# Kernel optimization log

Hardware: AMD Instinct MI355X
Metric: run time of the kernel (lower is better)

The kernel has to match this reference:

```python
import jax, jax.numpy as jnp
import numpy as np

N, K, DC, DH = 50000, 32, 64, 64  # nodes, neighbors, dim_c(+dim_h), dim_hidden

def setup_inputs() -> dict:
    key = jax.random.key(0)
    ks = jax.random.split(key, 8)
    return {
        "z":     jax.random.normal(ks[0], (N, DC), dtype=jnp.float32),
        "z_":    jax.random.normal(ks[1], (N, K, DC), dtype=jnp.float32),
        "W_cur": jax.random.normal(ks[2], (DC, DH), dtype=jnp.float32) * 0.1,
        "b_cur": jax.random.uniform(ks[3], (DH,), minval=-0.1, maxval=0.1, dtype=jnp.float32),
        "W_nbr": jax.random.normal(ks[4], (2 * DC, DH), dtype=jnp.float32) * 0.1,
        "b_nbr": jax.random.uniform(ks[5], (DH,), minval=-0.1, maxval=0.1, dtype=jnp.float32),
        "W_out": jax.random.normal(ks[6], (2 * DH, DC), dtype=jnp.float32) * 0.1,
        "b_out": jax.random.uniform(ks[7], (DC,), minval=-0.1, maxval=0.1, dtype=jnp.float32),
    }

def reference(z, z_, W_cur, b_cur, W_nbr, b_nbr, W_out, b_out):
    # cur branch: CELU(Linear(z))  -> [N, DH]
    v = jax.nn.celu(z @ W_cur + b_cur)
    # nbr branch: concat(self expanded over nbr axis, neighbors) -> [N, K, 2*DC]
    zz = jnp.concatenate((jnp.broadcast_to(z[:, None, :], z_.shape), z_), axis=-1)
    # CELU(Linear) then sum over neighbor axis -> [N, DH]
    v_ = jax.nn.celu(zz @ W_nbr + b_nbr).sum(axis=-2)
    # final linear on concatenated features -> [N, DC]
    dc = jnp.concatenate((v, v_), axis=-1) @ W_out + b_out
    return dc
```

## Files before the change

### kernel.cpp

```cpp
#include <hip/hip_runtime.h>
#include <hip/hip_bf16.h>

typedef float  f32x16 __attribute__((ext_vector_type(16)));
typedef short  bf16x8 __attribute__((ext_vector_type(8)));

__device__ __forceinline__ unsigned short f2bf(float x) {
  union { float f; unsigned u; } v; v.f = x;
  return (unsigned short)((v.u + 0x7FFFu + ((v.u >> 16) & 1u)) >> 16);
}

__device__ __forceinline__ float celu1(float x) {
  return x > 0.f ? x : (__expf(x) - 1.f);
}

struct Stage { float4 z[4][2]; float4 a[4][2]; };

__device__ __forceinline__ void issue_stage(Stage& s, const float* __restrict__ zptr,
                                            const float* __restrict__ aptr, int lo, int hi) {
#pragma unroll
  for (int ks = 0; ks < 4; ++ks) {
    const float* pz = zptr + ks * 16 + 8 * hi;
    s.z[ks][0] = *reinterpret_cast<const float4*>(pz);
    s.z[ks][1] = *reinterpret_cast<const float4*>(pz + 4);
    const float* pa = aptr + lo * 64 + ks * 16 + 8 * hi;
    s.a[ks][0] = *reinterpret_cast<const float4*>(pa);
    s.a[ks][1] = *reinterpret_cast<const float4*>(pa + 4);
  }
}

__device__ __forceinline__ bf16x8 to_frag(float4 a, float4 b) {
  bf16x8 r;
  r[0] = (short)f2bf(a.x); r[1] = (short)f2bf(a.y);
  r[2] = (short)f2bf(a.z); r[3] = (short)f2bf(a.w);
  r[4] = (short)f2bf(b.x); r[5] = (short)f2bf(b.y);
  r[6] = (short)f2bf(b.z); r[7] = (short)f2bf(b.w);
  return r;
}

__device__ __forceinline__ bf16x8 ldsfrag(const unsigned short* w, int S, int col, int k0) {
  return *reinterpret_cast<const bf16x8*>(w + col * S + (k0 ^ ((col & 7) << 3)));
}

__global__ __launch_bounds__(256, 2) void gcu_kernel(
    const float* __restrict__ z, const float* __restrict__ z_,
    const float* __restrict__ Wc, const float* __restrict__ bc,
    const float* __restrict__ Wn, const float* __restrict__ bn,
    const float* __restrict__ Wo, const float* __restrict__ bo,
    float* __restrict__ out, int N) {
  __shared__ __align__(16) unsigned short sWnT[64 * 128];
  __shared__ __align__(16) unsigned short sWcT[64 * 64];
  __shared__ __align__(16) unsigned short sWoT[64 * 128];
  __shared__ __align__(16) unsigned short sVV[4][32 * 128];

  const int tid = threadIdx.x;
  for (int i = tid; i < 128 * 64; i += 256) {
    int c = i & 63, k = i >> 6;
    int d = c * 128 + (k ^ ((c & 7) << 3));
    sWnT[d] = f2bf(Wn[i]);
    sWoT[d] = f2bf(Wo[i]);
  }
  for (int i = tid; i < 64 * 64; i += 256) {
    int c = i & 63, k = i >> 6;
    sWcT[c * 64 + (k ^ ((c & 7) << 3))] = f2bf(Wc[i]);
  }
  __syncthreads();

  const int wid = tid >> 6, lane = tid & 63;
  const int lo = lane & 31, hi = lane >> 5;
  const int base = (blockIdx.x * 4 + wid) * 32;
  if (base >= N) return;

  unsigned short* vv = &sVV[wid][0];
  const float bn0 = bn[lo], bn1 = bn[32 + lo];
  const float bc0 = bc[lo], bc1 = bc[32 + lo];
  const float bo0 = bo[lo], bo1 = bo[32 + lo];

  auto node_ptrs = [&](int n, const float*& zp, const float*& ap) {
    int nl = min(base + n, N - 1);
    zp = z + (size_t)nl * 64;
    ap = z_ + (size_t)nl * 2048;
  };

  auto process = [&](const Stage& s, int n) {
    f32x16 acc0{}, acc1{};
#pragma unroll
    for (int ks = 0; ks < 8; ++ks) {
      bf16x8 af = (ks < 4) ? to_frag(s.z[ks][0], s.z[ks][1])
                           : to_frag(s.a[ks - 4][0], s.a[ks - 4][1]);
      bf16x8 b0 = ldsfrag(sWnT, 128, lo,      ks * 16 + 8 * hi);
      bf16x8 b1 = ldsfrag(sWnT, 128, lo + 32, ks * 16 + 8 * hi);
      acc0 = __builtin_amdgcn_mfma_f32_32x32x16_bf16(af, b0, acc0, 0, 0, 0);
      acc1 = __builtin_amdgcn_mfma_f32_32x32x16_bf16(af, b1, acc1, 0, 0, 0);
    }
    float s0 = 0.f, s1 = 0.f;
#pragma unroll
    for (int r = 0; r < 16; ++r) {
      s0 += celu1(acc0[r] + bn0);
      s1 += celu1(acc1[r] + bn1);
    }
    s0 += __shfl_xor(s0, 32, 64);
    s1 += __shfl_xor(s1, 32, 64);
    if (hi == 0) {
      vv[n * 128 + ((64 + lo) ^ ((n & 7) << 3))] = f2bf(s0);
      vv[n * 128 + ((96 + lo) ^ ((n & 7) << 3))] = f2bf(s1);
    }
  };

  Stage sA, sB;
  { const float *zp, *ap; node_ptrs(0, zp, ap); issue_stage(sA, zp, ap, lo, hi); }
#pragma unroll 1
  for (int nn = 0; nn < 32; nn += 2) {
    const float *zp, *ap;
    node_ptrs(nn + 1, zp, ap);
    issue_stage(sB, zp, ap, lo, hi);
    process(sA, nn);
    node_ptrs(nn + 2, zp, ap);
    issue_stage(sA, zp, ap, lo, hi);
    process(sB, nn + 1);
  }

  {
    f32x16 a0{}, a1{};
    int nl = min(base + lo, N - 1);
    const float* zp = z + (size_t)nl * 64;
#pragma unroll
    for (int ks = 0; ks < 4; ++ks) {
      float4 x0 = *reinterpret_cast<const float4*>(zp + ks * 16 + 8 * hi);
      float4 x1 = *reinterpret_cast<const float4*>(zp + ks * 16 + 8 * hi + 4);
      bf16x8 af = to_frag(x0, x1);
      bf16x8 b0 = ldsfrag(sWcT, 64, lo,      ks * 16 + 8 * hi);
      bf16x8 b1 = ldsfrag(sWcT, 64, lo + 32, ks * 16 + 8 * hi);
      a0 = __builtin_amdgcn_mfma_f32_32x32x16_bf16(af, b0, a0, 0, 0, 0);
      a1 = __builtin_amdgcn_mfma_f32_32x32x16_bf16(af, b1, a1, 0, 0, 0);
    }
#pragma unroll
    for (int r = 0; r < 16; ++r) {
      int row = (r & 3) + 8 * (r >> 2) + 4 * hi;
      vv[row * 128 + ( lo        ^ ((row & 7) << 3))] = f2bf(celu1(a0[r] + bc0));
      vv[row * 128 + ((32 + lo)  ^ ((row & 7) << 3))] = f2bf(celu1(a1[r] + bc1));
    }
  }

  {
    f32x16 a0{}, a1{};
#pragma unroll
    for (int ks = 0; ks < 8; ++ks) {
      bf16x8 af = *reinterpret_cast<const bf16x8*>(
          vv + lo * 128 + ((ks * 16 + 8 * hi) ^ ((lo & 7) << 3)));
      bf16x8 b0 = ldsfrag(sWoT, 128, lo,      ks * 16 + 8 * hi);
      bf16x8 b1 = ldsfrag(sWoT, 128, lo + 32, ks * 16 + 8 * hi);
      a0 = __builtin_amdgcn_mfma_f32_32x32x16_bf16(af, b0, a0, 0, 0, 0);
      a1 = __builtin_amdgcn_mfma_f32_32x32x16_bf16(af, b1, a1, 0, 0, 0);
    }
#pragma unroll
    for (int r = 0; r < 16; ++r) {
      int row = base + (r & 3) + 8 * (r >> 2) + 4 * hi;
      if (row < N) {
        out[(size_t)row * 64 + lo]      = a0[r] + bo0;
        out[(size_t)row * 64 + 32 + lo] = a1[r] + bo1;
      }
    }
  }
}

extern "C" void kernel_launch(void* const* d_in, const int* in_sizes, int n_in,
                              void* d_out, int out_size, void* d_ws, size_t ws_size,
                              hipStream_t stream) {
  const float* z  = (const float*)d_in[0];
  const float* z_ = (const float*)d_in[1];
  const float* Wc = (const float*)d_in[2];
  const float* bc = (const float*)d_in[3];
  const float* Wn = (const float*)d_in[4];
  const float* bn = (const float*)d_in[5];
  const float* Wo = (const float*)d_in[6];
  const float* bo = (const float*)d_in[7];
  float* out = (float*)d_out;
  const int N = in_sizes[0] / 64;
  const int tasks = (N + 31) / 32;
  const int blocks = (tasks + 3) / 4;
  gcu_kernel<<<blocks, 256, 0, stream>>>(z, z_, Wc, bc, Wn, bn, Wo, bo, out, N);
}
```

Baseline: 109.3 us.

## Halve nodes per wave, shrink LDS, stage z in LDS, read Wc/Wo from global

Each wave now handles 16 nodes instead of 32, and launch bounds ask for three blocks per CU instead of two. To make room, only the neighbor weight stays in LDS, and the per-wave feature buffer is halved. The self features z are converted to bf16 once and staged in LDS, where both the neighbor GEMM and the cur branch read them. Wc and Wo fragments are now gathered straight from global memory with strided scalar loads. This cuts LDS use and per-thread staging registers to raise occupancy on the bandwidth-bound z_ stream. The cost is twice as many blocks, each repeating the Wn setup, plus uncoalesced global weight reads and half-used 32-row MFMA tiles in the final stages.

```diff
diff --git a/kernel.cpp b/kernel.cpp
--- a/kernel.cpp
+++ b/kernel.cpp
@@ -13,15 +13,12 @@
   return x > 0.f ? x : (__expf(x) - 1.f);
 }
 
-struct Stage { float4 z[4][2]; float4 a[4][2]; };
+struct Stage { float4 a[4][2]; };
 
-__device__ __forceinline__ void issue_stage(Stage& s, const float* __restrict__ zptr,
-                                            const float* __restrict__ aptr, int lo, int hi) {
+__device__ __forceinline__ void issue_stage(Stage& s, const float* __restrict__ aptr,
+                                            int lo, int hi) {
 #pragma unroll
   for (int ks = 0; ks < 4; ++ks) {
-    const float* pz = zptr + ks * 16 + 8 * hi;
-    s.z[ks][0] = *reinterpret_cast<const float4*>(pz);
-    s.z[ks][1] = *reinterpret_cast<const float4*>(pz + 4);
     const float* pa = aptr + lo * 64 + ks * 16 + 8 * hi;
     s.a[ks][0] = *reinterpret_cast<const float4*>(pa);
     s.a[ks][1] = *reinterpret_cast<const float4*>(pa + 4);
@@ -41,52 +38,67 @@
   return *reinterpret_cast<const bf16x8*>(w + col * S + (k0 ^ ((col & 7) << 3)));
 }
 
-__global__ __launch_bounds__(256, 2) void gcu_kernel(
+__device__ __forceinline__ bf16x8 wfrag(const float* __restrict__ W, int ld, int col, int k0) {
+  bf16x8 f;
+#pragma unroll
+  for (int j = 0; j < 8; ++j) f[j] = (short)f2bf(W[(size_t)(k0 + j) * ld + col]);
+  return f;
+}
+
+__global__ __launch_bounds__(256, 3) void gcu_kernel(
     const float* __restrict__ z, const float* __restrict__ z_,
     const float* __restrict__ Wc, const float* __restrict__ bc,
     const float* __restrict__ Wn, const float* __restrict__ bn,
     const float* __restrict__ Wo, const float* __restrict__ bo,
     float* __restrict__ out, int N) {
   __shared__ __align__(16) unsigned short sWnT[64 * 128];
-  __shared__ __align__(16) unsigned short sWcT[64 * 64];
-  __shared__ __align__(16) unsigned short sWoT[64 * 128];
-  __shared__ __align__(16) unsigned short sVV[4][32 * 128];
+  __shared__ __align__(16) unsigned short sVV[4][16 * 128];
 
   const int tid = threadIdx.x;
+  const int wid = tid >> 6, lane = tid & 63;
+  const int lo = lane & 31, hi = lane >> 5;
+  const int base = (blockIdx.x * 4 + wid) * 16;
+  unsigned short* vv = &sVV[wid][0];
+
   for (int i = tid; i < 128 * 64; i += 256) {
     int c = i & 63, k = i >> 6;
-    int d = c * 128 + (k ^ ((c & 7) << 3));
-    sWnT[d] = f2bf(Wn[i]);
-    sWoT[d] = f2bf(Wo[i]);
+    sWnT[c * 128 + (k ^ ((c & 7) << 3))] = f2bf(Wn[i]);
   }
-  for (int i = tid; i < 64 * 64; i += 256) {
-    int c = i & 63, k = i >> 6;
-    sWcT[c * 64 + (k ^ ((c & 7) << 3))] = f2bf(Wc[i]);
+
+  if (base < N) {
+    int r = lane >> 2, seg = lane & 3;
+    int node = min(base + r, N - 1);
+    const float* src = z + (size_t)node * 64 + seg * 16;
+    float4 x0 = *reinterpret_cast<const float4*>(src);
+    float4 x1 = *reinterpret_cast<const float4*>(src + 4);
+    float4 x2 = *reinterpret_cast<const float4*>(src + 8);
+    float4 x3 = *reinterpret_cast<const float4*>(src + 12);
+    int m = (r & 7) << 3;
+    *reinterpret_cast<bf16x8*>(vv + r * 128 + ((seg * 16)     ^ m)) = to_frag(x0, x1);
+    *reinterpret_cast<bf16x8*>(vv + r * 128 + ((seg * 16 + 8) ^ m)) = to_frag(x2, x3);
   }
   __syncthreads();
-
-  const int wid = tid >> 6, lane = tid & 63;
-  const int lo = lane & 31, hi = lane >> 5;
-  const int base = (blockIdx.x * 4 + wid) * 32;
   if (base >= N) return;
 
-  unsigned short* vv = &sVV[wid][0];
   const float bn0 = bn[lo], bn1 = bn[32 + lo];
   const float bc0 = bc[lo], bc1 = bc[32 + lo];
   const float bo0 = bo[lo], bo1 = bo[32 + lo];
 
-  auto node_ptrs = [&](int n, const float*& zp, const float*& ap) {
-    int nl = min(base + n, N - 1);
-    zp = z + (size_t)nl * 64;
-    ap = z_ + (size_t)nl * 2048;
+  auto aptr_of = [&](int n) {
+    return z_ + (size_t)min(base + n, N - 1) * 2048;
   };
 
   auto process = [&](const Stage& s, int n) {
     f32x16 acc0{}, acc1{};
 #pragma unroll
     for (int ks = 0; ks < 8; ++ks) {
-      bf16x8 af = (ks < 4) ? to_frag(s.z[ks][0], s.z[ks][1])
-                           : to_frag(s.a[ks - 4][0], s.a[ks - 4][1]);
+      bf16x8 af;
+      if (ks < 4) {
+        af = *reinterpret_cast<const bf16x8*>(
+            vv + n * 128 + ((ks * 16 + 8 * hi) ^ ((n & 7) << 3)));
+      } else {
+        af = to_frag(s.a[ks - 4][0], s.a[ks - 4][1]);
+      }
       bf16x8 b0 = ldsfrag(sWnT, 128, lo,      ks * 16 + 8 * hi);
       bf16x8 b1 = ldsfrag(sWnT, 128, lo + 32, ks * 16 + 8 * hi);
       acc0 = __builtin_amdgcn_mfma_f32_32x32x16_bf16(af, b0, acc0, 0, 0, 0);
@@ -107,34 +119,30 @@
   };
 
   Stage sA, sB;
-  { const float *zp, *ap; node_ptrs(0, zp, ap); issue_stage(sA, zp, ap, lo, hi); }
+  issue_stage(sA, aptr_of(0), lo, hi);
 #pragma unroll 1
-  for (int nn = 0; nn < 32; nn += 2) {
-    const float *zp, *ap;
-    node_ptrs(nn + 1, zp, ap);
-    issue_stage(sB, zp, ap, lo, hi);
+  for (int nn = 0; nn < 16; nn += 2) {
+    issue_stage(sB, aptr_of(nn + 1), lo, hi);
     process(sA, nn);
-    node_ptrs(nn + 2, zp, ap);
-    issue_stage(sA, zp, ap, lo, hi);
+    issue_stage(sA, aptr_of(nn + 2), lo, hi);
     process(sB, nn + 1);
   }
 
   {
     f32x16 a0{}, a1{};
-    int nl = min(base + lo, N - 1);
-    const float* zp = z + (size_t)nl * 64;
+    const int rl = lo & 15;
 #pragma unroll
     for (int ks = 0; ks < 4; ++ks) {
-      float4 x0 = *reinterpret_cast<const float4*>(zp + ks * 16 + 8 * hi);
-      float4 x1 = *reinterpret_cast<const float4*>(zp + ks * 16 + 8 * hi + 4);
-      bf16x8 af = to_frag(x0, x1);
-      bf16x8 b0 = ldsfrag(sWcT, 64, lo,      ks * 16 + 8 * hi);
-      bf16x8 b1 = ldsfrag(sWcT, 64, lo + 32, ks * 16 + 8 * hi);
+      int k0 = ks * 16 + 8 * hi;
+      bf16x8 af = *reinterpret_cast<const bf16x8*>(
+          vv + rl * 128 + (k0 ^ ((rl & 7) << 3)));
+      bf16x8 b0 = wfrag(Wc, 64, lo,      k0);
+      bf16x8 b1 = wfrag(Wc, 64, lo + 32, k0);
       a0 = __builtin_amdgcn_mfma_f32_32x32x16_bf16(af, b0, a0, 0, 0, 0);
       a1 = __builtin_amdgcn_mfma_f32_32x32x16_bf16(af, b1, a1, 0, 0, 0);
     }
 #pragma unroll
-    for (int r = 0; r < 16; ++r) {
+    for (int r = 0; r < 8; ++r) {
       int row = (r & 3) + 8 * (r >> 2) + 4 * hi;
       vv[row * 128 + ( lo        ^ ((row & 7) << 3))] = f2bf(celu1(a0[r] + bc0));
       vv[row * 128 + ((32 + lo)  ^ ((row & 7) << 3))] = f2bf(celu1(a1[r] + bc1));
@@ -143,17 +151,19 @@
 
   {
     f32x16 a0{}, a1{};
+    const int rl = lo & 15;
 #pragma unroll
     for (int ks = 0; ks < 8; ++ks) {
+      int k0 = ks * 16 + 8 * hi;
       bf16x8 af = *reinterpret_cast<const bf16x8*>(
-          vv + lo * 128 + ((ks * 16 + 8 * hi) ^ ((lo & 7) << 3)));
-      bf16x8 b0 = ldsfrag(sWoT, 128, lo,      ks * 16 + 8 * hi);
-      bf16x8 b1 = ldsfrag(sWoT, 128, lo + 32, ks * 16 + 8 * hi);
+          vv + rl * 128 + (k0 ^ ((rl & 7) << 3)));
+      bf16x8 b0 = wfrag(Wo, 64, lo,      k0);
+      bf16x8 b1 = wfrag(Wo, 64, lo + 32, k0);
       a0 = __builtin_amdgcn_mfma_f32_32x32x16_bf16(af, b0, a0, 0, 0, 0);
       a1 = __builtin_amdgcn_mfma_f32_32x32x16_bf16(af, b1, a1, 0, 0, 0);
     }
 #pragma unroll
-    for (int r = 0; r < 16; ++r) {
+    for (int r = 0; r < 8; ++r) {
       int row = base + (r & 3) + 8 * (r >> 2) + 4 * hi;
       if (row < N) {
         out[(size_t)row * 64 + lo]      = a0[r] + bo0;
@@ -176,7 +186,7 @@
   const float* bo = (const float*)d_in[7];
   float* out = (float*)d_out;
   const int N = in_sizes[0] / 64;
-  const int tasks = (N + 31) / 32;
+  const int tasks = (N + 15) / 16;
   const int blocks = (tasks + 3) / 4;
   gcu_kernel<<<blocks, 256, 0, stream>>>(z, z_, Wc, bc, Wn, bn, Wo, bo, out, N);
 }
```

After: 118.2 us. 1.08x slower.
